# Optimization experiments

Hardware: AMD Instinct MI355X
Metric: run time of the kernel (lower is better)

Reference implementation:

```python
import jax, jax.numpy as jnp
import numpy as np

B, L, D, H, F = 2, 1024, 1024, 16, 4096
DH = D // H
EPS = 1e-6


def _layernorm(x, g, b, eps=1e-5):
    m = jnp.mean(x, axis=-1, keepdims=True)
    v = jnp.mean((x - m) ** 2, axis=-1, keepdims=True)
    return (x - m) / jnp.sqrt(v + eps) * g + b


def setup_inputs() -> dict:
    key = jax.random.key(0)
    ks = jax.random.split(key, 12)

    def w(k, shape):
        return jax.random.normal(k, shape, dtype=jnp.float32) * 0.02

    return {
        "inputs": jax.random.normal(ks[0], (B, L, D), dtype=jnp.float32),
        "attn_mask": jnp.zeros((L, L), dtype=jnp.bool_),
        "Wq": w(ks[1], (D, D)), "bq": jnp.zeros((D,), jnp.float32),
        "Wk": w(ks[2], (D, D)), "bk": jnp.zeros((D,), jnp.float32),
        "Wv": w(ks[3], (D, D)), "bv": jnp.zeros((D,), jnp.float32),
        "Wo": w(ks[4], (D, D)), "bo": jnp.zeros((D,), jnp.float32),
        "ln1_g": jnp.ones((D,), jnp.float32), "ln1_b": jnp.zeros((D,), jnp.float32),
        "W1": w(ks[5], (D, F)), "b1": jnp.zeros((F,), jnp.float32),
        "W2": w(ks[6], (F, D)), "b2": jnp.zeros((D,), jnp.float32),
        "ln2_g": jnp.ones((D,), jnp.float32), "ln2_b": jnp.zeros((D,), jnp.float32),
    }


def _decoder_layer(inputs, Wq, bq, Wk, bk, Wv, bv, Wo, bo,
                   ln1_g, ln1_b, W1, b1, W2, b2, ln2_g, ln2_b):
    Bn, Ln, Dn = inputs.shape

    def heads(W, b):
        # [B,L,D] -> [B,H,L,Dh]
        return (inputs @ W + b).reshape(Bn, Ln, H, DH).transpose(0, 2, 1, 3)

    q = jax.nn.sigmoid(heads(Wq, bq))  # kernel feature map
    k = jax.nn.sigmoid(heads(Wk, bk))
    v = heads(Wv, bv)

    normal = (jnp.arange(Ln, dtype=jnp.float32) + 1.0)[None, None, :]  # [1,1,L]

    sink_in = normal / jnp.einsum('bhld,bhld->bhl', q + EPS, jnp.cumsum(k, axis=2) + EPS)
    src_out = normal / jnp.einsum('bhld,bhld->bhl', k + EPS, jnp.cumsum(q, axis=2) + EPS)

    cons_sink = jnp.einsum('bhld,bhld->bhl', q + EPS,
                           jnp.cumsum(k * src_out[..., None], axis=2) + EPS) / normal
    cons_src = jnp.einsum('bhld,bhld->bhl', k + EPS,
                          jnp.cumsum(q * sink_in[..., None], axis=2) + EPS) / normal
    cons_src = jnp.clip(cons_src, -1.0, 1.0)

    sink_alloc = jax.nn.sigmoid(cons_sink)
    cons_src = jnp.exp(cons_src)
    src_comp = cons_src / jnp.cumsum(cons_src, axis=-1) * normal

    # causal linear attention: cumsum of outer products k v^T, contracted with q
    qs = q * (sink_in / normal)[..., None]           # [B,H,L,Dh]
    vs = v * src_comp[..., None]                     # [B,H,L,Dh]
    kv = jnp.cumsum(jnp.einsum('bhld,bhlm->bhldm', k, vs), axis=2)  # [B,H,L,Dh,Dh]
    x = jnp.einsum('bhld,bhldm->bhlm', qs, kv) * sink_alloc[..., None]

    x = x.transpose(0, 2, 1, 3).reshape(Bn, Ln, Dn)
    attn = x @ Wo + bo

    h = _layernorm(inputs + attn, ln1_g, ln1_b)
    ffn = jax.nn.gelu(h @ W1 + b1, approximate=False) @ W2 + b2
    return _layernorm(h + ffn, ln2_g, ln2_b)


def reference(inputs, attn_mask, Wq, bq, Wk, bk, Wv, bv, Wo, bo,
              ln1_g, ln1_b, W1, b1, W2, b2, ln2_g, ln2_b):
    # attn_mask is unused by the original module (causality comes from cumsum)
    return _decoder_layer(inputs, Wq, bq, Wk, bk, Wv, bv, Wo, bo,
                          ln1_g, ln1_b, W1, b1, W2, b2, ln2_g, ln2_b)
```

## Files before the change

### kernel.cpp

```cpp
#include <hip/hip_runtime.h>
#include <hip/hip_bf16.h>

#define EPS 1e-6f
#define NBH 32
#define LSEQ 1024
#define DHD 64

typedef unsigned short u16;
typedef __bf16 bf16x8 __attribute__((ext_vector_type(8)));
typedef float f32x4 __attribute__((ext_vector_type(4)));

__device__ inline u16 f2bf(float f){
  union { float f; unsigned u; } un; un.f = f;
  unsigned u = un.u;
  u += 0x7fffu + ((u >> 16) & 1u);
  return (u16)(u >> 16);
}

__device__ inline float wred64(float v){
#pragma unroll
  for (int off = 32; off > 0; off >>= 1) v += __shfl_xor(v, off, 64);
  return v;
}

__device__ inline float wscan64(float v, int lane){
  float run = v;
#pragma unroll
  for (int off = 1; off < 64; off <<= 1){
    float t = __shfl_up(run, off, 64);
    if (lane >= off) run += t;
  }
  return run;
}

__device__ inline float fast_sigmoid(float x){
  return 1.f / (1.f + __expf(-x));
}

__device__ inline void gload_lds16(const u16* g, u16* l){
  __builtin_amdgcn_global_load_lds(
      (const __attribute__((address_space(1))) unsigned int*)g,
      (__attribute__((address_space(3))) unsigned int*)l, 16, 0, 0);
}

__device__ inline void tr_tile2(const float* in, u16* out, int R, int C, int r0, int c0){
  __shared__ float tile[32][33];
  int x = threadIdx.x & 31, y = threadIdx.x >> 5;
#pragma unroll
  for (int j = 0; j < 4; j++)
    tile[y + j*8][x] = in[(size_t)(r0 + y + j*8) * C + c0 + x];
  __syncthreads();
#pragma unroll
  for (int j = 0; j < 4; j++)
    out[(size_t)(c0 + y + j*8) * R + r0 + x] = f2bf(tile[x][y + j*8]);
}

__global__ __launch_bounds__(256) void prep_all(
    const float* __restrict__ inputs, u16* __restrict__ Xbf,
    const float* __restrict__ Wq, const float* __restrict__ Wk,
    const float* __restrict__ Wv, const float* __restrict__ Wo,
    u16* __restrict__ dqkv, u16* __restrict__ dwo,
    const float* __restrict__ W1, const float* __restrict__ W2,
    u16* __restrict__ d1, u16* __restrict__ d2,
    const float* __restrict__ bq, const float* __restrict__ bk,
    const float* __restrict__ bv, float* __restrict__ bqkv)
{
  int b = blockIdx.x;
  if (b < 2048){
    int i = b * 256 + threadIdx.x;
    float4 v = reinterpret_cast<const float4*>(inputs)[i];
    ushort4 o; o.x = f2bf(v.x); o.y = f2bf(v.y); o.z = f2bf(v.z); o.w = f2bf(v.w);
    reinterpret_cast<ushort4*>(Xbf)[i] = o;
  } else if (b < 6144){
    int t = b - 2048;
    int z = t >> 10, rem = t & 1023;
    int bx = rem & 31, by = rem >> 5;
    const float* in = (z == 0) ? Wq : (z == 1) ? Wk : (z == 2) ? Wv : Wo;
    u16* out = (z < 3) ? (dqkv + (size_t)z * 1024 * 1024) : dwo;
    tr_tile2(in, out, 1024, 1024, by * 32, bx * 32);
  } else if (b < 14336){
    int t = b - 6144;
    int z = t >> 12, rem = t & 4095;
    int bx = rem & 127, by = rem >> 7;
    if (z == 0) tr_tile2(W1, d1, 1024, 4096, by * 32, bx * 32);
    else        tr_tile2(W2, d2, 4096, 1024, bx * 32, by * 32);
  } else {
    int i = (b - 14336) * 256 + threadIdx.x;
    if (i < 3072){
      float v = (i < 1024) ? bq[i] : (i < 2048) ? bk[i - 1024] : bv[i - 2048];
      bqkv[i] = v;
    }
  }
}

template<int BM, int BN, int ACT, int OM>
__global__ __launch_bounds__(256) void gemm_mfma(
    const u16* __restrict__ A, const u16* __restrict__ Bt,
    const float* __restrict__ bias, const float* __restrict__ resid,
    float* __restrict__ outF, u16* __restrict__ outB,
    int M, int N, int K)
{
  constexpr int BK = 64;
  constexpr int MI = BM / 32;
  constexpr int NJ = BN / 32;
  constexpr int RA = BM / 32;
  constexpr int RB = BN / 32;
  constexpr int NS = RA + RB;
  __shared__ u16 As[2][BM * BK];
  __shared__ u16 Bs[2][BN * BK];
  const int tid = threadIdx.x;
  const int lane = tid & 63, wave = tid >> 6;
  const int lrow = lane & 15, lg = lane >> 4;
  const int m0 = blockIdx.x * BM, n0 = blockIdx.y * BN;
  const int wm = (wave >> 1) * (BM / 2), wn = (wave & 1) * (BN / 2);

  const int ksz = K / gridDim.z;
  const int k_begin = blockIdx.z * ksz;
  const int k_end = k_begin + ksz;

  f32x4 acc[MI][NJ];
#pragma unroll
  for (int i = 0; i < MI; i++)
#pragma unroll
    for (int j = 0; j < NJ; j++) acc[i][j] = (f32x4){0.f, 0.f, 0.f, 0.f};

  const u16* Ab = A + (size_t)m0 * K;
  const u16* Bb = Bt + (size_t)n0 * K;

  const int s0 = ((0 * 4 + lg) ^ (lrow & 7)) * 8;
  const int s1 = ((1 * 4 + lg) ^ (lrow & 7)) * 8;

  auto STAGE = [&](int buf, int k0){
#pragma unroll
    for (int r = 0; r < RA; ++r){
      int c = r * 256 + tid;
      int row = c >> 3;
      int kk = ((c ^ row) & 7) << 3;
      gload_lds16(Ab + (size_t)row * K + k0 + kk, &As[buf][(r * 256 + wave * 64) * 8]);
    }
#pragma unroll
    for (int r = 0; r < RB; ++r){
      int c = r * 256 + tid;
      int row = c >> 3;
      int kk = ((c ^ row) & 7) << 3;
      gload_lds16(Bb + (size_t)row * K + k0 + kk, &Bs[buf][(r * 256 + wave * 64) * 8]);
    }
  };

  STAGE(0, k_begin);
  int cur = 0;
  for (int k0 = k_begin; k0 < k_end; k0 += BK){
    if (k0 + BK < k_end){
      STAGE(cur ^ 1, k0 + BK);
      if constexpr (NS == 8)      asm volatile("s_waitcnt vmcnt(8)" ::: "memory");
      else if constexpr (NS == 6) asm volatile("s_waitcnt vmcnt(6)" ::: "memory");
      else                        asm volatile("s_waitcnt vmcnt(0)" ::: "memory");
    } else {
      asm volatile("s_waitcnt vmcnt(0)" ::: "memory");
    }
    __builtin_amdgcn_s_barrier();
    __builtin_amdgcn_sched_barrier(0);
#pragma unroll
    for (int kh = 0; kh < 2; ++kh){
      const int ss = (kh == 0) ? s0 : s1;
      bf16x8 af[MI], bfv[NJ];
#pragma unroll
      for (int i = 0; i < MI; ++i)
        af[i] = *reinterpret_cast<const bf16x8*>(&As[cur][(wm + i * 16 + lrow) * BK + ss]);
#pragma unroll
      for (int j = 0; j < NJ; ++j)
        bfv[j] = *reinterpret_cast<const bf16x8*>(&Bs[cur][(wn + j * 16 + lrow) * BK + ss]);
#pragma unroll
      for (int i = 0; i < MI; ++i)
#pragma unroll
        for (int j = 0; j < NJ; ++j)
          acc[i][j] = __builtin_amdgcn_mfma_f32_16x16x32_bf16(af[i], bfv[j], acc[i][j], 0, 0, 0);
    }
    __builtin_amdgcn_s_barrier();
    cur ^= 1;
  }

#pragma unroll
  for (int i = 0; i < MI; ++i){
#pragma unroll
    for (int j = 0; j < NJ; ++j){
      int col = n0 + wn + j * 16 + lrow;
      float bv = (OM != 4 && bias) ? bias[col] : 0.f;
#pragma unroll
      for (int r = 0; r < 4; ++r){
        int row = m0 + wm + i * 16 + lg * 4 + r;
        float x = acc[i][j][r] + bv;
        if (OM == 1){
          if (col < 2048) x = fast_sigmoid(x);
          int which = col >> 10, cc = col & 1023, h = cc >> 6, d = cc & 63;
          int b = row >> 10, l = row & 1023;
          outF[(size_t)which * (2048ull * 1024) +
               (((size_t)(b * 16 + h)) * 1024 + l) * 64 + d] = x;
        } else if (OM == 4){
          outF[((size_t)blockIdx.z * M + row) * N + col] = x;
        } else {
          if (ACT == 2){
            float u = 0.7978845608f * (x + 0.044715f * x * x * x);
            float e = __expf(2.f * u);
            x = 0.5f * x * (2.f - 2.f / (e + 1.f));
          }
          outB[(size_t)row * N + col] = f2bf(x);
        }
      }
    }
  }
}

__global__ __launch_bounds__(256) void chunk_sums(const float* __restrict__ k, const float* __restrict__ q,
                                                  float* __restrict__ ck, float* __restrict__ cq){
  int blk = blockIdx.x;
  int lane = threadIdx.x & 63, wave = threadIdx.x >> 6;
  size_t base = (size_t)blk * 64 * DHD;
  float sk = 0.f, sq = 0.f;
  for (int l = wave * 16; l < wave * 16 + 16; l++){
    sk += k[base + l * 64 + lane];
    sq += q[base + l * 64 + lane];
  }
  __shared__ float rd[2][4][64];
  rd[0][wave][lane] = sk; rd[1][wave][lane] = sq;
  __syncthreads();
  if (wave == 0){
    ck[(size_t)blk * 64 + lane] = rd[0][0][lane] + rd[0][1][lane] + rd[0][2][lane] + rd[0][3][lane];
    cq[(size_t)blk * 64 + lane] = rd[1][0][lane] + rd[1][1][lane] + rd[1][2][lane] + rd[1][3][lane];
  }
}

__global__ __launch_bounds__(256) void sink_tile(
    const float* __restrict__ q, const float* __restrict__ k,
    const float* __restrict__ ck, const float* __restrict__ cq,
    float* __restrict__ sink_in, float* __restrict__ src_out,
    float* __restrict__ cso, float* __restrict__ cqsi)
{
  int blk = blockIdx.x, bh = blk >> 4, c = blk & 15;
  int tid = threadIdx.x, lane = tid & 63, wave = tid >> 6;
  __shared__ float qT[64][65], kT[64][65], G[64][66];
  __shared__ float PK[64], PQ[64];
  __shared__ float rk[64], rq[64], crk[64], crq[64], siv[64], sov[64];
  __shared__ float rd[2][4][64];
  size_t base = ((size_t)bh * LSEQ + c * 64) * DHD;
  const float* qb = q + base; const float* kb = k + base;
  for (int c4 = tid; c4 < 1024; c4 += 256){
    int l = c4 >> 4, d0 = (c4 & 15) * 4;
    float4 qv = *reinterpret_cast<const float4*>(qb + c4 * 4);
    qT[d0+0][l] = qv.x; qT[d0+1][l] = qv.y; qT[d0+2][l] = qv.z; qT[d0+3][l] = qv.w;
    float4 kv = *reinterpret_cast<const float4*>(kb + c4 * 4);
    kT[d0+0][l] = kv.x; kT[d0+1][l] = kv.y; kT[d0+2][l] = kv.z; kT[d0+3][l] = kv.w;
  }
  if (tid < 64){
    float pk = 0.f, pq = 0.f;
    for (int cc = 0; cc < c; cc++){
      pk += ck[((size_t)bh * 16 + cc) * 64 + tid];
      pq += cq[((size_t)bh * 16 + cc) * 64 + tid];
    }
    PK[tid] = pk; PQ[tid] = pq;
  }
  __syncthreads();
  float sumPK = wred64(PK[lane]);
  float sumPQ = wred64(PQ[lane]);
  {
    int l = lane, g = wave;
    float qrow[64];
#pragma unroll
    for (int d = 0; d < 64; d++) qrow[d] = qT[d][l];
    float p[16] = {};
    for (int d = 0; d < 64; d++){
      float qv = qrow[d];
#pragma unroll
      for (int j4 = 0; j4 < 4; j4++){
        float4 kk = *reinterpret_cast<const float4*>(&kT[d][g * 16 + j4 * 4]);
        p[j4*4+0] += qv * kk.x; p[j4*4+1] += qv * kk.y;
        p[j4*4+2] += qv * kk.z; p[j4*4+3] += qv * kk.w;
      }
    }
#pragma unroll
    for (int jj = 0; jj < 16; jj++) G[l][g * 16 + jj] = p[jj];
  }
  {
    float pk_ = 0.f, pq_ = 0.f;
#pragma unroll
    for (int d = wave * 16; d < wave * 16 + 16; d++){
      pk_ += kT[d][lane]; pq_ += qT[d][lane];
    }
    rd[0][wave][lane] = pk_; rd[1][wave][lane] = pq_;
  }
  __syncthreads();
  if (tid < 64){
    rk[tid] = rd[0][0][tid] + rd[0][1][tid] + rd[0][2][tid] + rd[0][3][tid];
    rq[tid] = rd[1][0][tid] + rd[1][1][tid] + rd[1][2][tid] + rd[1][3][tid];
  }
  __syncthreads();
  if (wave == 0)      crk[lane] = wscan64(rk[lane], lane);
  else if (wave == 1) crq[lane] = wscan64(rq[lane], lane);
  __syncthreads();
  {
    int l = lane;
    float p1 = 0.f, p2 = 0.f;
#pragma unroll
    for (int j = wave * 16; j < wave * 16 + 16; j++){
      float g1 = (j <= l) ? G[l][j] : 0.f;
      p1 += g1 + qT[j][l] * PK[j];
      float g2 = (j <= l) ? G[j][l] : 0.f;
      p2 += g2 + kT[j][l] * PQ[j];
    }
    rd[0][wave][l] = p1; rd[1][wave][l] = p2;
  }
  __syncthreads();
  const float EPS2 = 64.f * EPS * EPS;
  if (tid < 64){
    int l = tid;
    float s1 = rd[0][0][l] + rd[0][1][l] + rd[0][2][l] + rd[0][3][l];
    float s2 = rd[1][0][l] + rd[1][1][l] + rd[1][2][l] + rd[1][3][l];
    int L = c * 64 + l; float nrm = (float)(L + 1);
    float den1 = s1 + EPS * rq[l] + EPS * (sumPK + crk[l]) + EPS2;
    float den2 = s2 + EPS * rk[l] + EPS * (sumPQ + crq[l]) + EPS2;
    float si_ = nrm / den1, so_ = nrm / den2;
    sink_in[(size_t)bh * LSEQ + L] = si_;
    src_out[(size_t)bh * LSEQ + L] = so_;
    siv[l] = si_; sov[l] = so_;
  }
  __syncthreads();
  float s1 = 0.f, s2 = 0.f;
  for (int l = wave * 16; l < wave * 16 + 16; l++){
    s1 += sov[l] * kT[lane][l];
    s2 += siv[l] * qT[lane][l];
  }
  rd[0][wave][lane] = s1; rd[1][wave][lane] = s2;
  __syncthreads();
  if (wave == 0){
    cso [(size_t)blk * 64 + lane] = rd[0][0][lane] + rd[0][1][lane] + rd[0][2][lane] + rd[0][3][lane];
    cqsi[(size_t)blk * 64 + lane] = rd[1][0][lane] + rd[1][1][lane] + rd[1][2][lane] + rd[1][3][lane];
  }
}

__global__ __launch_bounds__(256) void cons_tile(
    const float* __restrict__ q, const float* __restrict__ k,
    const float* __restrict__ cso, const float* __restrict__ cqsi,
    const float* __restrict__ sink_in, const float* __restrict__ src_out,
    float* __restrict__ sa, float* __restrict__ ebuf)
{
  int blk = blockIdx.x, bh = blk >> 4, c = blk & 15;
  int tid = threadIdx.x, lane = tid & 63, wave = tid >> 6;
  __shared__ float qT[64][65], kT[64][65], G[64][66];
  __shared__ float PKso[64], PQsi[64];
  __shared__ float rk[64], rq[64], cwrk[64], cwrq[64], siv[64], sov[64];
  __shared__ float rd[2][4][64];
  size_t base = ((size_t)bh * LSEQ + c * 64) * DHD;
  const float* qb = q + base; const float* kb = k + base;
  for (int c4 = tid; c4 < 1024; c4 += 256){
    int l = c4 >> 4, d0 = (c4 & 15) * 4;
    float4 qv = *reinterpret_cast<const float4*>(qb + c4 * 4);
    qT[d0+0][l] = qv.x; qT[d0+1][l] = qv.y; qT[d0+2][l] = qv.z; qT[d0+3][l] = qv.w;
    float4 kv = *reinterpret_cast<const float4*>(kb + c4 * 4);
    kT[d0+0][l] = kv.x; kT[d0+1][l] = kv.y; kT[d0+2][l] = kv.z; kT[d0+3][l] = kv.w;
  }
  if (tid < 64){
    float pk = 0.f, pq = 0.f;
    for (int cc = 0; cc < c; cc++){
      pk += cso [((size_t)bh * 16 + cc) * 64 + tid];
      pq += cqsi[((size_t)bh * 16 + cc) * 64 + tid];
    }
    PKso[tid] = pk; PQsi[tid] = pq;
  } else if (tid < 128){
    int l = tid - 64;
    sov[l] = src_out[(size_t)bh * LSEQ + c * 64 + l];
    siv[l] = sink_in[(size_t)bh * LSEQ + c * 64 + l];
  }
  __syncthreads();
  float sumPKso = wred64(PKso[lane]);
  float sumPQsi = wred64(PQsi[lane]);
  {
    int l = lane, g = wave;
    float qrow[64];
#pragma unroll
    for (int d = 0; d < 64; d++) qrow[d] = qT[d][l];
    float p[16] = {};
    for (int d = 0; d < 64; d++){
      float qv = qrow[d];
#pragma unroll
      for (int j4 = 0; j4 < 4; j4++){
        float4 kk = *reinterpret_cast<const float4*>(&kT[d][g * 16 + j4 * 4]);
        p[j4*4+0] += qv * kk.x; p[j4*4+1] += qv * kk.y;
        p[j4*4+2] += qv * kk.z; p[j4*4+3] += qv * kk.w;
      }
    }
#pragma unroll
    for (int jj = 0; jj < 16; jj++) G[l][g * 16 + jj] = p[jj];
  }
  {
    float pk_ = 0.f, pq_ = 0.f;
#pragma unroll
    for (int d = wave * 16; d < wave * 16 + 16; d++){
      pk_ += kT[d][lane]; pq_ += qT[d][lane];
    }
    rd[0][wave][lane] = pk_; rd[1][wave][lane] = pq_;
  }
  __syncthreads();
  if (tid < 64){
    rk[tid] = rd[0][0][tid] + rd[0][1][tid] + rd[0][2][tid] + rd[0][3][tid];
    rq[tid] = rd[1][0][tid] + rd[1][1][tid] + rd[1][2][tid] + rd[1][3][tid];
  }
  __syncthreads();
  if (wave == 0)      cwrk[lane] = wscan64(sov[lane] * rk[lane], lane);
  else if (wave == 1) cwrq[lane] = wscan64(siv[lane] * rq[lane], lane);
  __syncthreads();
  {
    int l = lane;
    float p3 = 0.f, p4 = 0.f;
#pragma unroll
    for (int j = wave * 16; j < wave * 16 + 16; j++){
      float g3 = (j <= l) ? sov[j] * G[l][j] : 0.f;
      p3 += g3 + qT[j][l] * PKso[j];
      float g4 = (j <= l) ? siv[j] * G[j][l] : 0.f;
      p4 += g4 + kT[j][l] * PQsi[j];
    }
    rd[0][wave][l] = p3; rd[1][wave][l] = p4;
  }
  __syncthreads();
  const float EPS2 = 64.f * EPS * EPS;
  if (tid < 64){
    int l = tid;
    float s3 = rd[0][0][l] + rd[0][1][l] + rd[0][2][l] + rd[0][3][l];
    float s4 = rd[1][0][l] + rd[1][1][l] + rd[1][2][l] + rd[1][3][l];
    int L = c * 64 + l; float nrm = (float)(L + 1);
    float cs = (s3 + EPS * rq[l] + EPS * (sumPKso + cwrk[l]) + EPS2) / nrm;
    sa[(size_t)bh * LSEQ + L] = fast_sigmoid(cs);
    float c2 = (s4 + EPS * rk[l] + EPS * (sumPQsi + cwrq[l]) + EPS2) / nrm;
    c2 = fminf(1.f, fmaxf(-1.f, c2));
    ebuf[(size_t)bh * LSEQ + L] = __expf(c2);
  }
}

__global__ __launch_bounds__(64) void srccomp_kernel(const float* __restrict__ ebuf, float* __restrict__ sc){
  int bh = blockIdx.x; int lane = threadIdx.x;
  const float* eb = ebuf + (size_t)bh * LSEQ;
  float loc[16]; float s = 0.f;
#pragma unroll
  for (int i = 0; i < 16; i++){ loc[i] = eb[lane * 16 + i]; s += loc[i]; }
  float run = wscan64(s, lane);
  float acc = run - s;
  float* scb = sc + (size_t)bh * LSEQ;
#pragma unroll
  for (int i = 0; i < 16; i++){
    acc += loc[i];
    scb[lane * 16 + i] = loc[i] / acc * (float)(lane * 16 + i + 1);
  }
}

__global__ __launch_bounds__(256) void phaseA(const float* __restrict__ k, const float* __restrict__ v,
                                              const float* __restrict__ sc, float* __restrict__ S){
  int blk = blockIdx.x; int bh = blk >> 4, c = blk & 15;
  __shared__ float ks[64][68], vss[64][68];
  __shared__ float vc[64];
  int tid = threadIdx.x;
  size_t base = ((size_t)bh * LSEQ + c * 64) * DHD;
  const float* kb = k + base; const float* vb = v + base;
  if (tid < 64) vc[tid] = sc[(size_t)bh * LSEQ + c * 64 + tid];
  __syncthreads();
  for (int c4 = tid; c4 < 1024; c4 += 256){
    int l = c4 >> 4, d0 = (c4 & 15) * 4;
    *reinterpret_cast<float4*>(&ks[l][d0]) = *reinterpret_cast<const float4*>(kb + c4 * 4);
    float4 vv = *reinterpret_cast<const float4*>(vb + c4 * 4);
    float w = vc[l];
    vss[l][d0+0] = vv.x * w; vss[l][d0+1] = vv.y * w;
    vss[l][d0+2] = vv.z * w; vss[l][d0+3] = vv.w * w;
  }
  __syncthreads();
  int m = tid >> 2, dg = tid & 3;
  float acc[16] = {};
  for (int l = 0; l < 64; l++){
    float vm = vss[l][m];
#pragma unroll
    for (int d4 = 0; d4 < 4; d4++){
      float4 kk = *reinterpret_cast<const float4*>(&ks[l][dg * 16 + d4 * 4]);
      acc[d4*4+0] += vm * kk.x; acc[d4*4+1] += vm * kk.y;
      acc[d4*4+2] += vm * kk.z; acc[d4*4+3] += vm * kk.w;
    }
  }
  float* Sb = S + (size_t)blk * 4096 + m * 64 + dg * 16;
#pragma unroll
  for (int d4 = 0; d4 < 4; d4++)
    *reinterpret_cast<float4*>(Sb + d4 * 4) =
        make_float4(acc[d4*4], acc[d4*4+1], acc[d4*4+2], acc[d4*4+3]);
}

__global__ __launch_bounds__(256) void phaseC(const float* __restrict__ q, const float* __restrict__ k,
                                              const float* __restrict__ v, const float* __restrict__ S,
                                              const float* __restrict__ sink_in, const float* __restrict__ sc,
                                              const float* __restrict__ sa, u16* __restrict__ x){
  int blk = blockIdx.x; int bh = blk >> 4, c = blk & 15;
  int b = bh >> 4, h = bh & 15;
  __shared__ float qp[64][66];
  __shared__ float kT[64][68];
  __shared__ float vss[64][68];
  __shared__ float kvs[64][68];
  __shared__ float qc[64], vc[64];
  int tid = threadIdx.x;
  size_t base = ((size_t)bh * LSEQ + c * 64) * DHD;
  const float* qb = q + base; const float* kb = k + base; const float* vb = v + base;
  if (tid < 64){
    int L = c * 64 + tid;
    qc[tid] = sink_in[(size_t)bh * LSEQ + L] / (float)(L + 1);
    vc[tid] = sc[(size_t)bh * LSEQ + L];
  }
  {
    int off16 = tid * 16;
    float accp[16] = {};
    for (int cc = 0; cc < c; cc++){
      size_t idx = ((size_t)bh * 16 + cc) * 4096 + off16;
#pragma unroll
      for (int t4 = 0; t4 < 4; t4++){
        float4 sv = *reinterpret_cast<const float4*>(S + idx + t4 * 4);
        accp[t4*4+0] += sv.x; accp[t4*4+1] += sv.y;
        accp[t4*4+2] += sv.z; accp[t4*4+3] += sv.w;
      }
    }
#pragma unroll
    for (int e = 0; e < 16; e++){
      int j = off16 + e;
      kvs[j >> 6][j & 63] = accp[e];
    }
  }
  __syncthreads();
  for (int c4 = tid; c4 < 1024; c4 += 256){
    int l = c4 >> 4, d0 = (c4 & 15) * 4;
    float qw = qc[l], vw = vc[l];
    float4 qv = *reinterpret_cast<const float4*>(qb + c4 * 4);
    qp[d0+0][l] = qv.x * qw; qp[d0+1][l] = qv.y * qw;
    qp[d0+2][l] = qv.z * qw; qp[d0+3][l] = qv.w * qw;
    float4 kv4 = *reinterpret_cast<const float4*>(kb + c4 * 4);
    kT[d0+0][l] = kv4.x; kT[d0+1][l] = kv4.y; kT[d0+2][l] = kv4.z; kT[d0+3][l] = kv4.w;
    float4 vv = *reinterpret_cast<const float4*>(vb + c4 * 4);
    vss[l][d0+0] = vv.x * vw; vss[l][d0+1] = vv.y * vw;
    vss[l][d0+2] = vv.z * vw; vss[l][d0+3] = vv.w * vw;
  }
  __syncthreads();
  int l = tid & 63, g = tid >> 6;
  float qrow[64];
#pragma unroll
  for (int d = 0; d < 64; d++) qrow[d] = qp[d][l];
  __syncthreads();

  float p[16] = {};
  for (int d = 0; d < 64; d++){
    float qv = qrow[d];
#pragma unroll
    for (int j4 = 0; j4 < 4; j4++){
      float4 kk = *reinterpret_cast<const float4*>(&kT[d][g * 16 + j4 * 4]);
      p[j4*4+0] += qv * kk.x; p[j4*4+1] += qv * kk.y;
      p[j4*4+2] += qv * kk.z; p[j4*4+3] += qv * kk.w;
    }
  }
#pragma unroll
  for (int jj = 0; jj < 16; jj++){
    int j = g * 16 + jj;
    qp[l][j] = (j <= l) ? p[jj] : 0.f;
  }
  __syncthreads();

  float acc[16];
#pragma unroll
  for (int mm = 0; mm < 16; mm++){
    float a = 0.f;
#pragma unroll
    for (int d4 = 0; d4 < 16; d4++){
      float4 kv4 = *reinterpret_cast<const float4*>(&kvs[g * 16 + mm][d4 * 4]);
      a += qrow[d4*4+0]*kv4.x + qrow[d4*4+1]*kv4.y + qrow[d4*4+2]*kv4.z + qrow[d4*4+3]*kv4.w;
    }
    acc[mm] = a;
  }
  for (int j = 0; j < 64; j++){
    float pv = qp[l][j];
#pragma unroll
    for (int m4 = 0; m4 < 4; m4++){
      float4 vv = *reinterpret_cast<const float4*>(&vss[j][g * 16 + m4 * 4]);
      acc[m4*4+0] += pv * vv.x; acc[m4*4+1] += pv * vv.y;
      acc[m4*4+2] += pv * vv.z; acc[m4*4+3] += pv * vv.w;
    }
  }
  float sav = sa[(size_t)bh * LSEQ + c * 64 + l];
  u16* xo = x + ((size_t)(b * 1024 + c * 64 + l)) * 1024 + h * 64 + g * 16;
#pragma unroll
  for (int mm = 0; mm < 16; mm++) xo[mm] = f2bf(acc[mm] * sav);
}

__global__ __launch_bounds__(256) void ln_fused2b(
    const float* __restrict__ p0, const float* __restrict__ p1,
    const float* __restrict__ resid, const float* __restrict__ bias,
    const float* __restrict__ g, const float* __restrict__ b,
    float* __restrict__ out, u16* __restrict__ outbf){
  int row = blockIdx.x; int tid = threadIdx.x;
  int lane = tid & 63, wave = tid >> 6;
  size_t off = (size_t)row * 1024 + tid * 4;
  float4 a0 = *reinterpret_cast<const float4*>(p0 + off);
  float4 a1 = *reinterpret_cast<const float4*>(p1 + off);
  float4 rr = *reinterpret_cast<const float4*>(resid + off);
  float4 bb = *reinterpret_cast<const float4*>(bias + tid * 4);
  float4 v = make_float4(a0.x + a1.x + rr.x + bb.x, a0.y + a1.y + rr.y + bb.y,
                         a0.z + a1.z + rr.z + bb.z, a0.w + a1.w + rr.w + bb.w);
  float s = v.x + v.y + v.z + v.w;
  float s2 = v.x*v.x + v.y*v.y + v.z*v.z + v.w*v.w;
  s = wred64(s); s2 = wred64(s2);
  __shared__ float red[2][4];
  if (lane == 0){ red[0][wave] = s; red[1][wave] = s2; }
  __syncthreads();
  float S = red[0][0] + red[0][1] + red[0][2] + red[0][3];
  float S2 = red[1][0] + red[1][1] + red[1][2] + red[1][3];
  float mean = S * (1.f / 1024.f);
  float var = S2 * (1.f / 1024.f) - mean * mean;
  float inv = rsqrtf(var + 1e-5f);
  float4 gv = *reinterpret_cast<const float4*>(g + tid * 4);
  float4 bv = *reinterpret_cast<const float4*>(b + tid * 4);
  float y0 = (v.x - mean) * inv * gv.x + bv.x;
  float y1 = (v.y - mean) * inv * gv.y + bv.y;
  float y2 = (v.z - mean) * inv * gv.z + bv.z;
  float y3 = (v.w - mean) * inv * gv.w + bv.w;
  *reinterpret_cast<float4*>(out + off) = make_float4(y0, y1, y2, y3);
  ushort4 o; o.x = f2bf(y0); o.y = f2bf(y1); o.z = f2bf(y2); o.w = f2bf(y3);
  *reinterpret_cast<ushort4*>(outbf + off) = o;
}

__global__ __launch_bounds__(256) void ln_fused4(
    const float* __restrict__ p0, const float* __restrict__ p1,
    const float* __restrict__ p2, const float* __restrict__ p3,
    const float* __restrict__ resid, const float* __restrict__ bias,
    const float* __restrict__ g, const float* __restrict__ b,
    float* __restrict__ out){
  int row = blockIdx.x; int tid = threadIdx.x;
  int lane = tid & 63, wave = tid >> 6;
  size_t off = (size_t)row * 1024 + tid * 4;
  float4 a0 = *reinterpret_cast<const float4*>(p0 + off);
  float4 a1 = *reinterpret_cast<const float4*>(p1 + off);
  float4 a2 = *reinterpret_cast<const float4*>(p2 + off);
  float4 a3 = *reinterpret_cast<const float4*>(p3 + off);
  float4 rr = *reinterpret_cast<const float4*>(resid + off);
  float4 bb = *reinterpret_cast<const float4*>(bias + tid * 4);
  float4 v = make_float4(a0.x + a1.x + a2.x + a3.x + rr.x + bb.x,
                         a0.y + a1.y + a2.y + a3.y + rr.y + bb.y,
                         a0.z + a1.z + a2.z + a3.z + rr.z + bb.z,
                         a0.w + a1.w + a2.w + a3.w + rr.w + bb.w);
  float s = v.x + v.y + v.z + v.w;
  float s2 = v.x*v.x + v.y*v.y + v.z*v.z + v.w*v.w;
  s = wred64(s); s2 = wred64(s2);
  __shared__ float red[2][4];
  if (lane == 0){ red[0][wave] = s; red[1][wave] = s2; }
  __syncthreads();
  float S = red[0][0] + red[0][1] + red[0][2] + red[0][3];
  float S2 = red[1][0] + red[1][1] + red[1][2] + red[1][3];
  float mean = S * (1.f / 1024.f);
  float var = S2 * (1.f / 1024.f) - mean * mean;
  float inv = rsqrtf(var + 1e-5f);
  float4 gv = *reinterpret_cast<const float4*>(g + tid * 4);
  float4 bv = *reinterpret_cast<const float4*>(b + tid * 4);
  float y0 = (v.x - mean) * inv * gv.x + bv.x;
  float y1 = (v.y - mean) * inv * gv.y + bv.y;
  float y2 = (v.z - mean) * inv * gv.z + bv.z;
  float y3 = (v.w - mean) * inv * gv.w + bv.w;
  *reinterpret_cast<float4*>(out + off) = make_float4(y0, y1, y2, y3);
}

extern "C" void kernel_launch(void* const* d_in, const int* in_sizes, int n_in,
                              void* d_out, int out_size, void* d_ws, size_t ws_size,
                              hipStream_t stream){
  (void)in_sizes; (void)n_in; (void)out_size; (void)ws_size;
  const float* inputs = (const float*)d_in[0];
  const float* Wq = (const float*)d_in[2];  const float* bq = (const float*)d_in[3];
  const float* Wk = (const float*)d_in[4];  const float* bk = (const float*)d_in[5];
  const float* Wv = (const float*)d_in[6];  const float* bv = (const float*)d_in[7];
  const float* Wo = (const float*)d_in[8];  const float* bo = (const float*)d_in[9];
  const float* ln1g = (const float*)d_in[10]; const float* ln1b = (const float*)d_in[11];
  const float* W1 = (const float*)d_in[12]; const float* b1 = (const float*)d_in[13];
  const float* W2 = (const float*)d_in[14]; const float* b2 = (const float*)d_in[15];
  const float* ln2g = (const float*)d_in[16]; const float* ln2b = (const float*)d_in[17];
  float* out = (float*)d_out;

  char* wsp = (char*)d_ws; size_t off = 0;
  auto alloc = [&](size_t bytes) -> void* {
    off = (off + 255) & ~(size_t)255;
    void* p = wsp + off; off += bytes; return p;
  };
  const size_t MD = (size_t)2048 * 1024;
  u16* Xbf    = (u16*)alloc(MD * 2);
  u16* WqkvT  = (u16*)alloc((size_t)3 * 1024 * 1024 * 2);
  u16* WoT    = (u16*)alloc((size_t)1024 * 1024 * 2);
  u16* W1T    = (u16*)alloc((size_t)4096 * 1024 * 2);
  u16* W2T    = (u16*)alloc((size_t)4096 * 1024 * 2);
  float* bqkv = (float*)alloc(3072 * 4);
  float* qkvb = (float*)alloc(3 * MD * 4);
  float* qb = qkvb; float* kb = qkvb + MD; float* vb = qkvb + 2 * MD;
  float* quad = (float*)alloc(4 * MD * 4);
  float* Sbuf = quad;
  float* ckb  = (float*)alloc((size_t)512 * 64 * 4);
  float* cqb  = (float*)alloc((size_t)512 * 64 * 4);
  float* csob = (float*)alloc((size_t)512 * 64 * 4);
  float* cqsib= (float*)alloc((size_t)512 * 64 * 4);
  float* sink_in = (float*)alloc(NBH * LSEQ * 4);
  float* src_out = (float*)alloc(NBH * LSEQ * 4);
  float* sabuf   = (float*)alloc(NBH * LSEQ * 4);
  float* ebuf    = (float*)alloc(NBH * LSEQ * 4);
  float* scbuf   = (float*)alloc(NBH * LSEQ * 4);
  u16* xatt   = (u16*)alloc(MD * 2);
  u16* g1     = (u16*)alloc((size_t)2048 * 4096 * 2);
  float* part = quad;
  float* hbuf = vb;
  u16* hbf = (u16*)qb;

  prep_all<<<14348, 256, 0, stream>>>(inputs, Xbf, Wq, Wk, Wv, Wo, WqkvT, WoT,
                                      W1, W2, W1T, W2T, bq, bk, bv, bqkv);

  gemm_mfma<128, 64, 0, 1><<<dim3(16, 48), 256, 0, stream>>>(
      Xbf, WqkvT, bqkv, nullptr, qkvb, nullptr, 2048, 3072, 1024);

  chunk_sums<<<512, 256, 0, stream>>>(kb, qb, ckb, cqb);
  sink_tile<<<512, 256, 0, stream>>>(qb, kb, ckb, cqb, sink_in, src_out, csob, cqsib);
  cons_tile<<<512, 256, 0, stream>>>(qb, kb, csob, cqsib, sink_in, src_out, sabuf, ebuf);
  srccomp_kernel<<<32, 64, 0, stream>>>(ebuf, scbuf);

  phaseA<<<512, 256, 0, stream>>>(kb, vb, scbuf, Sbuf);
  phaseC<<<512, 256, 0, stream>>>(qb, kb, vb, Sbuf, sink_in, scbuf, sabuf, xatt);

  float* wopart = quad + 2 * MD;
  gemm_mfma<128, 64, 0, 4><<<dim3(16, 16, 2), 256, 0, stream>>>(
      xatt, WoT, nullptr, nullptr, wopart, nullptr, 2048, 1024, 1024);
  ln_fused2b<<<2048, 256, 0, stream>>>(wopart, wopart + MD, inputs, bo, ln1g, ln1b, hbuf, hbf);

  gemm_mfma<128, 128, 2, 3><<<dim3(16, 32), 256, 0, stream>>>(
      hbf, W1T, b1, nullptr, nullptr, g1, 2048, 4096, 1024);
  gemm_mfma<128, 128, 0, 4><<<dim3(16, 8, 4), 256, 0, stream>>>(
      g1, W2T, nullptr, nullptr, part, nullptr, 2048, 1024, 4096);
  ln_fused4<<<2048, 256, 0, stream>>>(part, part + MD, part + 2 * MD, part + 3 * MD,
                                      hbuf, b2, ln2g, ln2b, out);
}
```

Measured before the change: 198.9 us.

## Fuse chunk sums into QKV GEMM epilogue and store W2 split-K partials as bf16

The separate chunk_sums kernel is removed. Per-chunk column sums of sigmoid(q) and sigmoid(k) are now accumulated in the QKV GEMM epilogue and written with atomicAdd into buffers that prep_all zeroes beforehand. Separately, the W2 split-K GEMM writes its partial results in bf16 instead of fp32, and the final layernorm reads bf16 partials. This avoids re-reading q/k and halves partial-sum traffic. In exchange it adds atomic contention and some precision loss, and the zeroing relies on the ck and cq buffers being contiguous in memory.

Measured after the change: 195.6 us. Within noise of the previous version (-1.7%).

```diff
diff --git a/kernel.cpp b/kernel.cpp
--- a/kernel.cpp
+++ b/kernel.cpp
@@ -15,6 +15,10 @@
   unsigned u = un.u;
   u += 0x7fffu + ((u >> 16) & 1u);
   return (u16)(u >> 16);
+}
+
+__device__ inline float bf2f(u16 v){
+  union { unsigned u; float f; } un; un.u = ((unsigned)v) << 16; return un.f;
 }
 
 __device__ inline float wred64(float v){
@@ -63,7 +67,8 @@
     const float* __restrict__ W1, const float* __restrict__ W2,
     u16* __restrict__ d1, u16* __restrict__ d2,
     const float* __restrict__ bq, const float* __restrict__ bk,
-    const float* __restrict__ bv, float* __restrict__ bqkv)
+    const float* __restrict__ bv, float* __restrict__ bqkv,
+    float* __restrict__ ckq_zero)
 {
   int b = blockIdx.x;
   if (b < 2048){
@@ -84,12 +89,15 @@
     int bx = rem & 127, by = rem >> 7;
     if (z == 0) tr_tile2(W1, d1, 1024, 4096, by * 32, bx * 32);
     else        tr_tile2(W2, d2, 4096, 1024, bx * 32, by * 32);
-  } else {
+  } else if (b < 14348){
     int i = (b - 14336) * 256 + threadIdx.x;
     if (i < 3072){
       float v = (i < 1024) ? bq[i] : (i < 2048) ? bk[i - 1024] : bv[i - 2048];
       bqkv[i] = v;
     }
+  } else {
+    int i = (b - 14348) * 256 + threadIdx.x;
+    reinterpret_cast<float4*>(ckq_zero)[i] = make_float4(0.f, 0.f, 0.f, 0.f);
   }
 }
 
@@ -98,6 +106,7 @@
     const u16* __restrict__ A, const u16* __restrict__ Bt,
     const float* __restrict__ bias, const float* __restrict__ resid,
     float* __restrict__ outF, u16* __restrict__ outB,
+    float* __restrict__ cqA, float* __restrict__ ckA,
     int M, int N, int K)
 {
   constexpr int BK = 64;
@@ -180,24 +189,30 @@
     cur ^= 1;
   }
 
+  float csum[NJ];
+#pragma unroll
+  for (int j = 0; j < NJ; ++j) csum[j] = 0.f;
+
 #pragma unroll
   for (int i = 0; i < MI; ++i){
 #pragma unroll
     for (int j = 0; j < NJ; ++j){
       int col = n0 + wn + j * 16 + lrow;
-      float bv = (OM != 4 && bias) ? bias[col] : 0.f;
+      float bv = (OM < 4 && bias) ? bias[col] : 0.f;
 #pragma unroll
       for (int r = 0; r < 4; ++r){
         int row = m0 + wm + i * 16 + lg * 4 + r;
         float x = acc[i][j][r] + bv;
         if (OM == 1){
-          if (col < 2048) x = fast_sigmoid(x);
+          if (col < 2048){ x = fast_sigmoid(x); csum[j] += x; }
           int which = col >> 10, cc = col & 1023, h = cc >> 6, d = cc & 63;
           int b = row >> 10, l = row & 1023;
           outF[(size_t)which * (2048ull * 1024) +
                (((size_t)(b * 16 + h)) * 1024 + l) * 64 + d] = x;
         } else if (OM == 4){
           outF[((size_t)blockIdx.z * M + row) * N + col] = x;
+        } else if (OM == 5){
+          outB[((size_t)blockIdx.z * M + row) * N + col] = f2bf(x);
         } else {
           if (ACT == 2){
             float u = 0.7978845608f * (x + 0.044715f * x * x * x);
@@ -209,24 +224,19 @@
       }
     }
   }
-}
-
-__global__ __launch_bounds__(256) void chunk_sums(const float* __restrict__ k, const float* __restrict__ q,
-                                                  float* __restrict__ ck, float* __restrict__ cq){
-  int blk = blockIdx.x;
-  int lane = threadIdx.x & 63, wave = threadIdx.x >> 6;
-  size_t base = (size_t)blk * 64 * DHD;
-  float sk = 0.f, sq = 0.f;
-  for (int l = wave * 16; l < wave * 16 + 16; l++){
-    sk += k[base + l * 64 + lane];
-    sq += q[base + l * 64 + lane];
-  }
-  __shared__ float rd[2][4][64];
-  rd[0][wave][lane] = sk; rd[1][wave][lane] = sq;
-  __syncthreads();
-  if (wave == 0){
-    ck[(size_t)blk * 64 + lane] = rd[0][0][lane] + rd[0][1][lane] + rd[0][2][lane] + rd[0][3][lane];
-    cq[(size_t)blk * 64 + lane] = rd[1][0][lane] + rd[1][1][lane] + rd[1][2][lane] + rd[1][3][lane];
+  if (OM == 1){
+#pragma unroll
+    for (int j = 0; j < NJ; ++j){
+      int col = n0 + wn + j * 16 + lrow;
+      if (col < 2048){
+        int which = col >> 10, cc = col & 1023, h = cc >> 6, d = cc & 63;
+        int rowbase = m0 + wm;
+        int bh = (rowbase >> 10) * 16 + h;
+        int chunk = (rowbase & 1023) >> 6;
+        float* dst = (which == 0) ? cqA : ckA;
+        atomicAdd(&dst[((size_t)bh * 16 + chunk) * 64 + d], csum[j]);
+      }
+    }
   }
 }
 
@@ -624,25 +634,26 @@
   *reinterpret_cast<ushort4*>(outbf + off) = o;
 }
 
-__global__ __launch_bounds__(256) void ln_fused4(
-    const float* __restrict__ p0, const float* __restrict__ p1,
-    const float* __restrict__ p2, const float* __restrict__ p3,
+__global__ __launch_bounds__(256) void ln_fused4b(
+    const u16* __restrict__ p0, const u16* __restrict__ p1,
+    const u16* __restrict__ p2, const u16* __restrict__ p3,
     const float* __restrict__ resid, const float* __restrict__ bias,
     const float* __restrict__ g, const float* __restrict__ b,
     float* __restrict__ out){
   int row = blockIdx.x; int tid = threadIdx.x;
   int lane = tid & 63, wave = tid >> 6;
   size_t off = (size_t)row * 1024 + tid * 4;
-  float4 a0 = *reinterpret_cast<const float4*>(p0 + off);
-  float4 a1 = *reinterpret_cast<const float4*>(p1 + off);
-  float4 a2 = *reinterpret_cast<const float4*>(p2 + off);
-  float4 a3 = *reinterpret_cast<const float4*>(p3 + off);
+  ushort4 u0 = *reinterpret_cast<const ushort4*>(p0 + off);
+  ushort4 u1 = *reinterpret_cast<const ushort4*>(p1 + off);
+  ushort4 u2 = *reinterpret_cast<const ushort4*>(p2 + off);
+  ushort4 u3 = *reinterpret_cast<const ushort4*>(p3 + off);
   float4 rr = *reinterpret_cast<const float4*>(resid + off);
   float4 bb = *reinterpret_cast<const float4*>(bias + tid * 4);
-  float4 v = make_float4(a0.x + a1.x + a2.x + a3.x + rr.x + bb.x,
-                         a0.y + a1.y + a2.y + a3.y + rr.y + bb.y,
-                         a0.z + a1.z + a2.z + a3.z + rr.z + bb.z,
-                         a0.w + a1.w + a2.w + a3.w + rr.w + bb.w);
+  float4 v = make_float4(
+      bf2f(u0.x) + bf2f(u1.x) + bf2f(u2.x) + bf2f(u3.x) + rr.x + bb.x,
+      bf2f(u0.y) + bf2f(u1.y) + bf2f(u2.y) + bf2f(u3.y) + rr.y + bb.y,
+      bf2f(u0.z) + bf2f(u1.z) + bf2f(u2.z) + bf2f(u3.z) + rr.z + bb.z,
+      bf2f(u0.w) + bf2f(u1.w) + bf2f(u2.w) + bf2f(u3.w) + rr.w + bb.w);
   float s = v.x + v.y + v.z + v.w;
   float s2 = v.x*v.x + v.y*v.y + v.z*v.z + v.w*v.w;
   s = wred64(s); s2 = wred64(s2);
@@ -705,17 +716,16 @@
   float* scbuf   = (float*)alloc(NBH * LSEQ * 4);
   u16* xatt   = (u16*)alloc(MD * 2);
   u16* g1     = (u16*)alloc((size_t)2048 * 4096 * 2);
-  float* part = quad;
+  u16* partb  = (u16*)quad;
   float* hbuf = vb;
   u16* hbf = (u16*)qb;
 
-  prep_all<<<14348, 256, 0, stream>>>(inputs, Xbf, Wq, Wk, Wv, Wo, WqkvT, WoT,
-                                      W1, W2, W1T, W2T, bq, bk, bv, bqkv);
+  prep_all<<<14412, 256, 0, stream>>>(inputs, Xbf, Wq, Wk, Wv, Wo, WqkvT, WoT,
+                                      W1, W2, W1T, W2T, bq, bk, bv, bqkv, ckb);
 
   gemm_mfma<128, 64, 0, 1><<<dim3(16, 48), 256, 0, stream>>>(
-      Xbf, WqkvT, bqkv, nullptr, qkvb, nullptr, 2048, 3072, 1024);
-
-  chunk_sums<<<512, 256, 0, stream>>>(kb, qb, ckb, cqb);
+      Xbf, WqkvT, bqkv, nullptr, qkvb, nullptr, cqb, ckb, 2048, 3072, 1024);
+
   sink_tile<<<512, 256, 0, stream>>>(qb, kb, ckb, cqb, sink_in, src_out, csob, cqsib);
   cons_tile<<<512, 256, 0, stream>>>(qb, kb, csob, cqsib, sink_in, src_out, sabuf, ebuf);
   srccomp_kernel<<<32, 64, 0, stream>>>(ebuf, scbuf);
@@ -725,13 +735,13 @@
 
   float* wopart = quad + 2 * MD;
   gemm_mfma<128, 64, 0, 4><<<dim3(16, 16, 2), 256, 0, stream>>>(
-      xatt, WoT, nullptr, nullptr, wopart, nullptr, 2048, 1024, 1024);
+      xatt, WoT, nullptr, nullptr, wopart, nullptr, nullptr, nullptr, 2048, 1024, 1024);
   ln_fused2b<<<2048, 256, 0, stream>>>(wopart, wopart + MD, inputs, bo, ln1g, ln1b, hbuf, hbf);
 
   gemm_mfma<128, 128, 2, 3><<<dim3(16, 32), 256, 0, stream>>>(
-      hbf, W1T, b1, nullptr, nullptr, g1, 2048, 4096, 1024);
-  gemm_mfma<128, 128, 0, 4><<<dim3(16, 8, 4), 256, 0, stream>>>(
-      g1, W2T, nullptr, nullptr, part, nullptr, 2048, 1024, 4096);
-  ln_fused4<<<2048, 256, 0, stream>>>(part, part + MD, part + 2 * MD, part + 3 * MD,
-                                      hbuf, b2, ln2g, ln2b, out);
-}
+      hbf, W1T, b1, nullptr, nullptr, g1, nullptr, nullptr, 2048, 4096, 1024);
+  gemm_mfma<128, 128, 0, 5><<<dim3(16, 8, 4), 256, 0, stream>>>(
+      g1, W2T, nullptr, nullptr, nullptr, partb, nullptr, nullptr, 2048, 1024, 4096);
+  ln_fused4b<<<2048, 256, 0, stream>>>(partb, partb + MD, partb + 2 * MD, partb + 3 * MD,
+                                       hbuf, b2, ln2g, ln2b, out);
+}
```
